# Optimization experiments

Measured on AMD Instinct MI355X. Metric: run time of the kernel, lower is better.

The kernel has to match this reference:

```python
import jax, jax.numpy as jnp
import numpy as np

PREV_SIZE = 1024
SIZE = 4096
BATCH = 8192


def setup_inputs() -> dict:
    key = jax.random.key(0)
    k1, k2, k3, k4 = jax.random.split(key, 4)
    return {
        "prev_layer_output": jax.random.normal(k1, (PREV_SIZE, BATCH), dtype=jnp.float32),
        "input_A_weights": jax.random.normal(k2, (SIZE, PREV_SIZE), dtype=jnp.float32),
        "input_B_weights": jax.random.normal(k3, (SIZE, PREV_SIZE), dtype=jnp.float32),
        "table_weights": jax.random.normal(k4, (16, SIZE), dtype=jnp.float32),
    }


def reference(prev_layer_output, input_A_weights, input_B_weights, table_weights):
    # Soft input selection via row-softmax over previous neurons.
    pa = jax.nn.softmax(input_A_weights, axis=1)   # (size, prev_size)
    pb = jax.nn.softmax(input_B_weights, axis=1)   # (size, prev_size)
    pt = jax.nn.softmax(table_weights, axis=0)     # (16, size) softmax over gates

    A = pa @ prev_layer_output                     # (size, batch)
    B = pb @ prev_layer_output                     # (size, batch)
    AB = A * B

    p = pt[:, :, None]                             # (16, size, 1) broadcast over batch
    # Fused weighted sum over the 16 soft logic gates (no (16,size,batch) buffer).
    out = (
        p[1] * AB
        + p[2] * (A - AB)
        + p[3] * A
        + p[4] * (B - AB)
        + p[5] * B
        + p[6] * (A + B - 2.0 * AB)
        + p[7] * (A + B - AB)
        + p[8] * (1.0 - (A + B - AB))
        + p[9] * (1.0 - (A + B - 2.0 * AB))
        + p[10] * (1.0 - B)
        + p[11] * (1.0 - B + AB)
        + p[12] * (1.0 - A)
        + p[13] * (1.0 - A + AB)
        + p[14] * (1.0 - AB)
        + p[15]
    )
    return out
```

## Files before the change

### kernel.cpp

```cpp
#include <hip/hip_runtime.h>
#include <hip/hip_bf16.h>

#define K_DIM 1024
#define M_DIM 4096
#define N_DIM 8192
#define BK 32
#define PAD 40

typedef __attribute__((ext_vector_type(8))) __bf16 bf16x8_t;
typedef __attribute__((ext_vector_type(4))) float f32x4;
typedef __attribute__((ext_vector_type(4))) int i32x4;

__device__ inline unsigned short f2bf(float f) {
    unsigned u = __float_as_uint(f);
    u += 0x7FFF + ((u >> 16) & 1);
    return (unsigned short)(u >> 16);
}

__global__ void row_softmax_kernel(const float* __restrict__ w,
                                   unsigned short* __restrict__ o) {
    const int row = blockIdx.x;
    const int tid = threadIdx.x;
    const float4 v = reinterpret_cast<const float4*>(w + (size_t)row * K_DIM)[tid];
    float m = fmaxf(fmaxf(v.x, v.y), fmaxf(v.z, v.w));
    #pragma unroll
    for (int off = 32; off >= 1; off >>= 1) m = fmaxf(m, __shfl_xor(m, off));
    __shared__ float redm[4];
    __shared__ float reds[4];
    if ((tid & 63) == 0) redm[tid >> 6] = m;
    __syncthreads();
    m = fmaxf(fmaxf(redm[0], redm[1]), fmaxf(redm[2], redm[3]));
    const float e0 = __expf(v.x - m), e1 = __expf(v.y - m);
    const float e2 = __expf(v.z - m), e3 = __expf(v.w - m);
    float s = e0 + e1 + e2 + e3;
    #pragma unroll
    for (int off = 32; off >= 1; off >>= 1) s += __shfl_xor(s, off);
    if ((tid & 63) == 0) reds[tid >> 6] = s;
    __syncthreads();
    s = reds[0] + reds[1] + reds[2] + reds[3];
    const float inv = 1.0f / s;
    ushort4 r;
    r.x = f2bf(e0 * inv); r.y = f2bf(e1 * inv);
    r.z = f2bf(e2 * inv); r.w = f2bf(e3 * inv);
    reinterpret_cast<ushort4*>(o + (size_t)row * K_DIM)[tid] = r;
}

__global__ void transpose_conv_kernel(const float* __restrict__ src,
                                      unsigned short* __restrict__ dst) {
    __shared__ float t[32][33];
    const int n0 = blockIdx.x * 32;
    const int k0 = blockIdx.y * 32;
    const int tx = threadIdx.x, ty = threadIdx.y;
    #pragma unroll
    for (int i = ty; i < 32; i += 8)
        t[i][tx] = src[(size_t)(k0 + i) * N_DIM + n0 + tx];
    __syncthreads();
    #pragma unroll
    for (int i = ty; i < 32; i += 8)
        dst[(size_t)(n0 + i) * K_DIM + k0 + tx] = f2bf(t[tx][i]);
}

__global__ void coef_kernel(const float* __restrict__ tw,
                            float4* __restrict__ coef) {
    const int r = blockIdx.x * 256 + threadIdx.x;
    float p[16];
    float m = -1e30f;
    #pragma unroll
    for (int k = 0; k < 16; ++k) { p[k] = tw[k * M_DIM + r]; m = fmaxf(m, p[k]); }
    float s = 0.f;
    #pragma unroll
    for (int k = 0; k < 16; ++k) { p[k] = __expf(p[k] - m); s += p[k]; }
    const float inv = 1.f / s;
    #pragma unroll
    for (int k = 0; k < 16; ++k) p[k] *= inv;
    const float cA  = p[2]+p[3]+p[6]+p[7]-p[8]-p[9]-p[12]-p[13];
    const float cB  = p[4]+p[5]+p[6]+p[7]-p[8]-p[9]-p[10]-p[11];
    const float cAB = p[1]-p[2]-p[4]-2.f*p[6]-p[7]+p[8]+2.f*p[9]+p[11]+p[13]-p[14];
    const float c0  = p[8]+p[9]+p[10]+p[11]+p[12]+p[13]+p[14]+p[15];
    coef[r] = make_float4(cA, cB, cAB, c0);
}

__global__ __launch_bounds__(256, 2)
void dual_gemm_kernel(const unsigned short* __restrict__ pa,
                      const unsigned short* __restrict__ pb,
                      const unsigned short* __restrict__ pv,
                      const float4* __restrict__ coef,
                      float* __restrict__ out) {
    __shared__ unsigned short sA[128 * PAD];
    __shared__ unsigned short sB[128 * PAD];
    __shared__ unsigned short sP[128 * PAD];

    const int tid = threadIdx.x;
    const int lane = tid & 63;
    const int wid = tid >> 6;
    const int wm = wid >> 1, wn = wid & 1;
    const int bm = blockIdx.y, bn = blockIdx.x;

    f32x4 accA[4][4], accB[4][4];
    const f32x4 z = {0.f, 0.f, 0.f, 0.f};
    #pragma unroll
    for (int i = 0; i < 4; ++i)
        #pragma unroll
        for (int j = 0; j < 4; ++j) { accA[i][j] = z; accB[i][j] = z; }

    const size_t a_base = (size_t)(bm * 128) * K_DIM;
    const size_t p_base = (size_t)(bn * 128) * K_DIM;

    const int frag_row = lane & 15;
    const int frag_k = (lane >> 4) * 8;

    for (int k0 = 0; k0 < K_DIM; k0 += BK) {
        __syncthreads();
        #pragma unroll
        for (int i = 0; i < 2; ++i) {
            const int c = tid + i * 256;
            const int r = c >> 2;
            const int kk = (c & 3) * 8;
            *reinterpret_cast<i32x4*>(&sA[r * PAD + kk]) =
                *reinterpret_cast<const i32x4*>(&pa[a_base + (size_t)r * K_DIM + k0 + kk]);
            *reinterpret_cast<i32x4*>(&sB[r * PAD + kk]) =
                *reinterpret_cast<const i32x4*>(&pb[a_base + (size_t)r * K_DIM + k0 + kk]);
            *reinterpret_cast<i32x4*>(&sP[r * PAD + kk]) =
                *reinterpret_cast<const i32x4*>(&pv[p_base + (size_t)r * K_DIM + k0 + kk]);
        }
        __syncthreads();

        bf16x8_t af[4], bfr[4], pf[4];
        #pragma unroll
        for (int mi = 0; mi < 4; ++mi) {
            const int row = wm * 64 + mi * 16 + frag_row;
            af[mi]  = *reinterpret_cast<const bf16x8_t*>(&sA[row * PAD + frag_k]);
            bfr[mi] = *reinterpret_cast<const bf16x8_t*>(&sB[row * PAD + frag_k]);
        }
        #pragma unroll
        for (int ni = 0; ni < 4; ++ni) {
            const int col = wn * 64 + ni * 16 + frag_row;
            pf[ni] = *reinterpret_cast<const bf16x8_t*>(&sP[col * PAD + frag_k]);
        }
        #pragma unroll
        for (int mi = 0; mi < 4; ++mi)
            #pragma unroll
            for (int ni = 0; ni < 4; ++ni) {
                accA[mi][ni] = __builtin_amdgcn_mfma_f32_16x16x32_bf16(
                    af[mi], pf[ni], accA[mi][ni], 0, 0, 0);
                accB[mi][ni] = __builtin_amdgcn_mfma_f32_16x16x32_bf16(
                    bfr[mi], pf[ni], accB[mi][ni], 0, 0, 0);
            }
    }

    const int row_grp = lane >> 4;
    #pragma unroll
    for (int mi = 0; mi < 4; ++mi) {
        #pragma unroll
        for (int ni = 0; ni < 4; ++ni) {
            const int gr0 = bm * 128 + wm * 64 + mi * 16 + row_grp * 4;
            const int gc  = bn * 128 + wn * 64 + ni * 16 + (lane & 15);
            #pragma unroll
            for (int i = 0; i < 4; ++i) {
                const int r = gr0 + i;
                const float4 cf = coef[r];
                const float av = accA[mi][ni][i];
                const float bv = accB[mi][ni][i];
                out[(size_t)r * N_DIM + gc] =
                    fmaf(cf.z, av * bv, fmaf(cf.x, av, fmaf(cf.y, bv, cf.w)));
            }
        }
    }
}

extern "C" void kernel_launch(void* const* d_in, const int* in_sizes, int n_in,
                              void* d_out, int out_size, void* d_ws, size_t ws_size,
                              hipStream_t stream) {
    const float* prev = (const float*)d_in[0];
    const float* wa   = (const float*)d_in[1];
    const float* wb   = (const float*)d_in[2];
    const float* tw   = (const float*)d_in[3];
    float* out = (float*)d_out;

    char* ws = (char*)d_ws;
    unsigned short* pa = (unsigned short*)ws;
    unsigned short* pb = (unsigned short*)(ws + 8388608);
    unsigned short* pv = (unsigned short*)(ws + 16777216);
    float4* coef       = (float4*)(ws + 33554432);

    row_softmax_kernel<<<M_DIM, 256, 0, stream>>>(wa, pa);
    row_softmax_kernel<<<M_DIM, 256, 0, stream>>>(wb, pb);
    transpose_conv_kernel<<<dim3(N_DIM / 32, K_DIM / 32), dim3(32, 8), 0, stream>>>(prev, pv);
    coef_kernel<<<M_DIM / 256, 256, 0, stream>>>(tw, coef);
    dual_gemm_kernel<<<dim3(N_DIM / 128, M_DIM / 128), 256, 0, stream>>>(pa, pb, pv, coef, out);
}
```

Measured before the change: 179.9 us.

## Load GEMM tiles with direct global-to-LDS copies, XOR swizzle, and BK=64

Replaces the register-staged global-to-shared tile copies with global_load_lds direct-to-LDS 16-byte loads. The shared-memory layout changes from padded rows to an XOR-swizzled 128-byte row layout to avoid bank conflicts. The K tile is doubled to 64, which halves the number of barrier pairs per K sweep. The change removes VGPR staging and load/store instruction overhead, but it relies on the per-wave LDS destination addressing of the builtin being correct and enlarges shared memory per block.

After: 150.2 us. 16.5% less time.

```diff
diff --git a/kernel.cpp b/kernel.cpp
--- a/kernel.cpp
+++ b/kernel.cpp
@@ -4,17 +4,21 @@
 #define K_DIM 1024
 #define M_DIM 4096
 #define N_DIM 8192
-#define BK 32
-#define PAD 40
+#define BK 64
 
 typedef __attribute__((ext_vector_type(8))) __bf16 bf16x8_t;
 typedef __attribute__((ext_vector_type(4))) float f32x4;
-typedef __attribute__((ext_vector_type(4))) int i32x4;
 
 __device__ inline unsigned short f2bf(float f) {
     unsigned u = __float_as_uint(f);
     u += 0x7FFF + ((u >> 16) & 1);
     return (unsigned short)(u >> 16);
+}
+
+__device__ __forceinline__ void gload_lds16(const void* g, void* l) {
+    __builtin_amdgcn_global_load_lds(
+        (const __attribute__((address_space(1))) unsigned int*)g,
+        (__attribute__((address_space(3))) unsigned int*)l, 16, 0, 0);
 }
 
 __global__ void row_softmax_kernel(const float* __restrict__ w,
@@ -86,9 +90,9 @@
                       const unsigned short* __restrict__ pv,
                       const float4* __restrict__ coef,
                       float* __restrict__ out) {
-    __shared__ unsigned short sA[128 * PAD];
-    __shared__ unsigned short sB[128 * PAD];
-    __shared__ unsigned short sP[128 * PAD];
+    __shared__ unsigned short sA[128 * BK];
+    __shared__ unsigned short sB[128 * BK];
+    __shared__ unsigned short sP[128 * BK];
 
     const int tid = threadIdx.x;
     const int lane = tid & 63;
@@ -103,49 +107,59 @@
         #pragma unroll
         for (int j = 0; j < 4; ++j) { accA[i][j] = z; accB[i][j] = z; }
 
-    const size_t a_base = (size_t)(bm * 128) * K_DIM;
-    const size_t p_base = (size_t)(bn * 128) * K_DIM;
+    const int sub_row = lane >> 3;
+    const int scol16  = (lane & 7) ^ sub_row;
 
     const int frag_row = lane & 15;
-    const int frag_k = (lane >> 4) * 8;
+    const int fk16base = lane >> 4;
 
     for (int k0 = 0; k0 < K_DIM; k0 += BK) {
         __syncthreads();
         #pragma unroll
-        for (int i = 0; i < 2; ++i) {
-            const int c = tid + i * 256;
-            const int r = c >> 2;
-            const int kk = (c & 3) * 8;
-            *reinterpret_cast<i32x4*>(&sA[r * PAD + kk]) =
-                *reinterpret_cast<const i32x4*>(&pa[a_base + (size_t)r * K_DIM + k0 + kk]);
-            *reinterpret_cast<i32x4*>(&sB[r * PAD + kk]) =
-                *reinterpret_cast<const i32x4*>(&pb[a_base + (size_t)r * K_DIM + k0 + kk]);
-            *reinterpret_cast<i32x4*>(&sP[r * PAD + kk]) =
-                *reinterpret_cast<const i32x4*>(&pv[p_base + (size_t)r * K_DIM + k0 + kk]);
+        for (int j = 0; j < 4; ++j) {
+            const int c   = wid * 4 + j;
+            const int row = c * 8 + sub_row;
+            const size_t goffA = (size_t)(bm * 128 + row) * K_DIM + k0;
+            const size_t goffP = (size_t)(bn * 128 + row) * K_DIM + k0;
+            const char* gA = (const char*)(pa + goffA) + scol16 * 16;
+            const char* gB = (const char*)(pb + goffA) + scol16 * 16;
+            const char* gP = (const char*)(pv + goffP) + scol16 * 16;
+            char* lA = (char*)sA + c * 1024;
+            char* lB = (char*)sB + c * 1024;
+            char* lP = (char*)sP + c * 1024;
+            gload_lds16(gA, lA);
+            gload_lds16(gB, lB);
+            gload_lds16(gP, lP);
         }
         __syncthreads();
 
-        bf16x8_t af[4], bfr[4], pf[4];
-        #pragma unroll
-        for (int mi = 0; mi < 4; ++mi) {
-            const int row = wm * 64 + mi * 16 + frag_row;
-            af[mi]  = *reinterpret_cast<const bf16x8_t*>(&sA[row * PAD + frag_k]);
-            bfr[mi] = *reinterpret_cast<const bf16x8_t*>(&sB[row * PAD + frag_k]);
+        #pragma unroll
+        for (int kk = 0; kk < 2; ++kk) {
+            bf16x8_t af[4], bfr[4], pf[4];
+            const int fk16 = fk16base + kk * 4;
+            #pragma unroll
+            for (int mi = 0; mi < 4; ++mi) {
+                const int row  = wm * 64 + mi * 16 + frag_row;
+                const int byte = row * 128 + ((fk16 ^ (row & 7)) * 16);
+                af[mi]  = *reinterpret_cast<const bf16x8_t*>((const char*)sA + byte);
+                bfr[mi] = *reinterpret_cast<const bf16x8_t*>((const char*)sB + byte);
+            }
+            #pragma unroll
+            for (int ni = 0; ni < 4; ++ni) {
+                const int col  = wn * 64 + ni * 16 + frag_row;
+                const int byte = col * 128 + ((fk16 ^ (col & 7)) * 16);
+                pf[ni] = *reinterpret_cast<const bf16x8_t*>((const char*)sP + byte);
+            }
+            #pragma unroll
+            for (int mi = 0; mi < 4; ++mi)
+                #pragma unroll
+                for (int ni = 0; ni < 4; ++ni) {
+                    accA[mi][ni] = __builtin_amdgcn_mfma_f32_16x16x32_bf16(
+                        af[mi], pf[ni], accA[mi][ni], 0, 0, 0);
+                    accB[mi][ni] = __builtin_amdgcn_mfma_f32_16x16x32_bf16(
+                        bfr[mi], pf[ni], accB[mi][ni], 0, 0, 0);
+                }
         }
-        #pragma unroll
-        for (int ni = 0; ni < 4; ++ni) {
-            const int col = wn * 64 + ni * 16 + frag_row;
-            pf[ni] = *reinterpret_cast<const bf16x8_t*>(&sP[col * PAD + frag_k]);
-        }
-        #pragma unroll
-        for (int mi = 0; mi < 4; ++mi)
-            #pragma unroll
-            for (int ni = 0; ni < 4; ++ni) {
-                accA[mi][ni] = __builtin_amdgcn_mfma_f32_16x16x32_bf16(
-                    af[mi], pf[ni], accA[mi][ni], 0, 0, 0);
-                accB[mi][ni] = __builtin_amdgcn_mfma_f32_16x16x32_bf16(
-                    bfr[mi], pf[ni], accB[mi][ni], 0, 0, 0);
-            }
     }
 
     const int row_grp = lane >> 4;
```

## Pipeline GEMM with triple-buffered direct-to-LDS loads and XOR-swizzled layout

Applied to the files above, without the earlier changes.

Rewrites the dual GEMM main loop to stage tiles with global_load_lds directly into a triple-buffered, XOR-swizzled LDS layout. Loads run two stages ahead, synchronised with explicit vmcnt/lgkmcnt waits and one barrier per iteration, and MFMA priority is raised. This is meant to hide global memory latency and remove register round-trips and bank conflicts. The two row-softmax launches are also merged into one. LDS use rises to 72KB, which may limit occupancy to two blocks per CU.

Measured after the change: 163.4 us. 1.1x faster.

```diff
diff --git a/kernel.cpp b/kernel.cpp
--- a/kernel.cpp
+++ b/kernel.cpp
@@ -5,11 +5,25 @@
 #define M_DIM 4096
 #define N_DIM 8192
 #define BK 32
-#define PAD 40
+#define BM 128
+#define BN 128
+#define NT 32
+
+#define OFF_A 0
+#define OFF_B 8192
+#define OFF_P 16384
+#define BUF_BYTES 24576
 
 typedef __attribute__((ext_vector_type(8))) __bf16 bf16x8_t;
 typedef __attribute__((ext_vector_type(4))) float f32x4;
-typedef __attribute__((ext_vector_type(4))) int i32x4;
+
+#define SBAR do { __builtin_amdgcn_sched_barrier(0); \
+                  __builtin_amdgcn_s_barrier(); \
+                  __builtin_amdgcn_sched_barrier(0); } while (0)
+#define LGKM0 do { asm volatile("s_waitcnt lgkmcnt(0)" ::: "memory"); \
+                   __builtin_amdgcn_sched_barrier(0); } while (0)
+#define VMCNT(n) do { asm volatile("s_waitcnt vmcnt(" #n ")" ::: "memory"); \
+                      __builtin_amdgcn_sched_barrier(0); } while (0)
 
 __device__ inline unsigned short f2bf(float f) {
     unsigned u = __float_as_uint(f);
@@ -17,9 +31,20 @@
     return (unsigned short)(u >> 16);
 }
 
-__global__ void row_softmax_kernel(const float* __restrict__ w,
-                                   unsigned short* __restrict__ o) {
-    const int row = blockIdx.x;
+__device__ __forceinline__ void gload_lds16(const void* g, void* l) {
+    __builtin_amdgcn_global_load_lds(
+        (const __attribute__((address_space(1))) unsigned int*)g,
+        (__attribute__((address_space(3))) unsigned int*)l, 16, 0, 0);
+}
+
+__global__ void dual_softmax_kernel(const float* __restrict__ wa,
+                                    const float* __restrict__ wb,
+                                    unsigned short* __restrict__ pa,
+                                    unsigned short* __restrict__ pb) {
+    const int idx = blockIdx.x;
+    const float* w = (idx < M_DIM) ? wa : wb;
+    unsigned short* o = (idx < M_DIM) ? pa : pb;
+    const int row = idx & (M_DIM - 1);
     const int tid = threadIdx.x;
     const float4 v = reinterpret_cast<const float4*>(w + (size_t)row * K_DIM)[tid];
     float m = fmaxf(fmaxf(v.x, v.y), fmaxf(v.z, v.w));
@@ -86,15 +111,29 @@
                       const unsigned short* __restrict__ pv,
                       const float4* __restrict__ coef,
                       float* __restrict__ out) {
-    __shared__ unsigned short sA[128 * PAD];
-    __shared__ unsigned short sB[128 * PAD];
-    __shared__ unsigned short sP[128 * PAD];
+    __shared__ unsigned short lds[3 * BUF_BYTES / 2];
 
     const int tid = threadIdx.x;
     const int lane = tid & 63;
-    const int wid = tid >> 6;
-    const int wm = wid >> 1, wn = wid & 1;
+    const int w = tid >> 6;
+    const int wm = w >> 1, wn = w & 1;
     const int bm = blockIdx.y, bn = blockIdx.x;
+
+    const int sub  = lane >> 2;
+    const int scol = (lane & 3) ^ ((lane >> 3) & 3);
+
+    const int c0 = w * 2, c1 = w * 2 + 1;
+    const char* sA0 = (const char*)pa + ((size_t)(bm * BM + c0 * 16 + sub) * K_DIM) * 2 + scol * 16;
+    const char* sA1 = (const char*)pa + ((size_t)(bm * BM + c1 * 16 + sub) * K_DIM) * 2 + scol * 16;
+    const char* sB0 = (const char*)pb + ((size_t)(bm * BM + c0 * 16 + sub) * K_DIM) * 2 + scol * 16;
+    const char* sB1 = (const char*)pb + ((size_t)(bm * BM + c1 * 16 + sub) * K_DIM) * 2 + scol * 16;
+    const char* sP0 = (const char*)pv + ((size_t)(bn * BN + c0 * 16 + sub) * K_DIM) * 2 + scol * 16;
+    const char* sP1 = (const char*)pv + ((size_t)(bn * BN + c1 * 16 + sub) * K_DIM) * 2 + scol * 16;
+
+    const int fr  = lane & 15;
+    const int fk  = lane >> 4;
+    const int arow0 = wm * 64 + fr;
+    const int prow0 = wn * 64 + fr;
 
     f32x4 accA[4][4], accB[4][4];
     const f32x4 z = {0.f, 0.f, 0.f, 0.f};
@@ -103,49 +142,79 @@
         #pragma unroll
         for (int j = 0; j < 4; ++j) { accA[i][j] = z; accB[i][j] = z; }
 
-    const size_t a_base = (size_t)(bm * 128) * K_DIM;
-    const size_t p_base = (size_t)(bn * 128) * K_DIM;
-
-    const int frag_row = lane & 15;
-    const int frag_k = (lane >> 4) * 8;
-
-    for (int k0 = 0; k0 < K_DIM; k0 += BK) {
-        __syncthreads();
-        #pragma unroll
-        for (int i = 0; i < 2; ++i) {
-            const int c = tid + i * 256;
-            const int r = c >> 2;
-            const int kk = (c & 3) * 8;
-            *reinterpret_cast<i32x4*>(&sA[r * PAD + kk]) =
-                *reinterpret_cast<const i32x4*>(&pa[a_base + (size_t)r * K_DIM + k0 + kk]);
-            *reinterpret_cast<i32x4*>(&sB[r * PAD + kk]) =
-                *reinterpret_cast<const i32x4*>(&pb[a_base + (size_t)r * K_DIM + k0 + kk]);
-            *reinterpret_cast<i32x4*>(&sP[r * PAD + kk]) =
-                *reinterpret_cast<const i32x4*>(&pv[p_base + (size_t)r * K_DIM + k0 + kk]);
+    #define STAGE_ALL(bo) do {                                              \
+        char* base = (char*)lds + (bo);                                     \
+        gload_lds16(sA0, base + OFF_A + c0 * 1024);                         \
+        gload_lds16(sA1, base + OFF_A + c1 * 1024);                         \
+        gload_lds16(sB0, base + OFF_B + c0 * 1024);                         \
+        gload_lds16(sB1, base + OFF_B + c1 * 1024);                         \
+        gload_lds16(sP0, base + OFF_P + c0 * 1024);                         \
+        gload_lds16(sP1, base + OFF_P + c1 * 1024);                         \
+        sA0 += BK * 2; sA1 += BK * 2; sB0 += BK * 2; sB1 += BK * 2;         \
+        sP0 += BK * 2; sP1 += BK * 2;                                       \
+    } while (0)
+
+    #define READ_FRAGS(bo)                                                   \
+        bf16x8_t af[4], bfv[4], pf[4];                                       \
+        {                                                                    \
+            const char* base = (const char*)lds + (bo);                      \
+            _Pragma("unroll")                                                \
+            for (int mi = 0; mi < 4; ++mi) {                                 \
+                const int row = arow0 + mi * 16;                             \
+                const int byte = row * 64 + ((fk ^ ((row >> 1) & 3)) << 4);  \
+                af[mi]  = *reinterpret_cast<const bf16x8_t*>(base + OFF_A + byte); \
+                bfv[mi] = *reinterpret_cast<const bf16x8_t*>(base + OFF_B + byte); \
+            }                                                                \
+            _Pragma("unroll")                                                \
+            for (int ni = 0; ni < 4; ++ni) {                                 \
+                const int row = prow0 + ni * 16;                             \
+                const int byte = row * 64 + ((fk ^ ((row >> 1) & 3)) << 4);  \
+                pf[ni] = *reinterpret_cast<const bf16x8_t*>(base + OFF_P + byte); \
+            }                                                                \
         }
-        __syncthreads();
-
-        bf16x8_t af[4], bfr[4], pf[4];
-        #pragma unroll
-        for (int mi = 0; mi < 4; ++mi) {
-            const int row = wm * 64 + mi * 16 + frag_row;
-            af[mi]  = *reinterpret_cast<const bf16x8_t*>(&sA[row * PAD + frag_k]);
-            bfr[mi] = *reinterpret_cast<const bf16x8_t*>(&sB[row * PAD + frag_k]);
-        }
-        #pragma unroll
-        for (int ni = 0; ni < 4; ++ni) {
-            const int col = wn * 64 + ni * 16 + frag_row;
-            pf[ni] = *reinterpret_cast<const bf16x8_t*>(&sP[col * PAD + frag_k]);
-        }
-        #pragma unroll
-        for (int mi = 0; mi < 4; ++mi)
-            #pragma unroll
-            for (int ni = 0; ni < 4; ++ni) {
-                accA[mi][ni] = __builtin_amdgcn_mfma_f32_16x16x32_bf16(
-                    af[mi], pf[ni], accA[mi][ni], 0, 0, 0);
-                accB[mi][ni] = __builtin_amdgcn_mfma_f32_16x16x32_bf16(
-                    bfr[mi], pf[ni], accB[mi][ni], 0, 0, 0);
-            }
+
+    #define MFMA_ALL do {                                                    \
+        __builtin_amdgcn_s_setprio(1);                                       \
+        _Pragma("unroll")                                                    \
+        for (int mi = 0; mi < 4; ++mi)                                       \
+            _Pragma("unroll")                                                \
+            for (int ni = 0; ni < 4; ++ni) {                                 \
+                accA[mi][ni] = __builtin_amdgcn_mfma_f32_16x16x32_bf16(      \
+                    af[mi], pf[ni], accA[mi][ni], 0, 0, 0);                  \
+                accB[mi][ni] = __builtin_amdgcn_mfma_f32_16x16x32_bf16(      \
+                    bfv[mi], pf[ni], accB[mi][ni], 0, 0, 0);                 \
+            }                                                                \
+        __builtin_amdgcn_s_setprio(0);                                       \
+    } while (0)
+
+    STAGE_ALL(0);
+    STAGE_ALL(BUF_BYTES);
+    VMCNT(6);
+    SBAR;
+
+    int curb = 0, stgb = 2 * BUF_BYTES;
+    for (int t = 0; t < NT - 2; ++t) {
+        STAGE_ALL(stgb);
+        READ_FRAGS(curb);
+        LGKM0;
+        MFMA_ALL;
+        VMCNT(6);
+        SBAR;
+        stgb = curb;
+        curb = (curb == 2 * BUF_BYTES) ? 0 : curb + BUF_BYTES;
+    }
+    {
+        READ_FRAGS(curb);
+        LGKM0;
+        MFMA_ALL;
+        VMCNT(0);
+        SBAR;
+        curb = (curb == 2 * BUF_BYTES) ? 0 : curb + BUF_BYTES;
+    }
+    {
+        READ_FRAGS(curb);
+        LGKM0;
+        MFMA_ALL;
     }
 
     const int row_grp = lane >> 4;
@@ -153,8 +222,8 @@
     for (int mi = 0; mi < 4; ++mi) {
         #pragma unroll
         for (int ni = 0; ni < 4; ++ni) {
-            const int gr0 = bm * 128 + wm * 64 + mi * 16 + row_grp * 4;
-            const int gc  = bn * 128 + wn * 64 + ni * 16 + (lane & 15);
+            const int gr0 = bm * BM + wm * 64 + mi * 16 + row_grp * 4;
+            const int gc  = bn * BN + wn * 64 + ni * 16 + (lane & 15);
             #pragma unroll
             for (int i = 0; i < 4; ++i) {
                 const int r = gr0 + i;
@@ -183,9 +252,8 @@
     unsigned short* pv = (unsigned short*)(ws + 16777216);
     float4* coef       = (float4*)(ws + 33554432);
 
-    row_softmax_kernel<<<M_DIM, 256, 0, stream>>>(wa, pa);
-    row_softmax_kernel<<<M_DIM, 256, 0, stream>>>(wb, pb);
+    dual_softmax_kernel<<<2 * M_DIM, 256, 0, stream>>>(wa, wb, pa, pb);
     transpose_conv_kernel<<<dim3(N_DIM / 32, K_DIM / 32), dim3(32, 8), 0, stream>>>(prev, pv);
     coef_kernel<<<M_DIM / 256, 256, 0, stream>>>(tw, coef);
-    dual_gemm_kernel<<<dim3(N_DIM / 128, M_DIM / 128), 256, 0, stream>>>(pa, pb, pv, coef, out);
-}
+    dual_gemm_kernel<<<dim3(N_DIM / BN, M_DIM / BM), 256, 0, stream>>>(pa, pb, pv, coef, out);
+}
```

## Double-buffer GEMM tiles via direct global-to-LDS loads with XOR swizzle

Applied to the files above, without the earlier changes.

The dual GEMM now stages tiles straight from global memory into LDS using global_load_lds, with two LDS buffers so the next k-tile loads while the current one feeds the MFMAs. An XOR swizzle replaces the padded layout to avoid bank conflicts, and s_setprio raises priority around the MFMA block. The two row-softmax launches are also merged into one kernel. This trades a more intricate sync scheme (vmcnt waits plus a barrier) and double the LDS footprint for fewer register round-trips and less exposed load latency.

Measured after the change: 164.0 us. 1.1x faster.

```diff
diff --git a/kernel.cpp b/kernel.cpp
--- a/kernel.cpp
+++ b/kernel.cpp
@@ -5,11 +5,20 @@
 #define M_DIM 4096
 #define N_DIM 8192
 #define BK 32
-#define PAD 40
+#define BM 128
+#define BN 128
+#define NT 32
+
+#define OFF_A 0
+#define OFF_B 8192
+#define OFF_P 16384
+#define BUF_BYTES 24576
 
 typedef __attribute__((ext_vector_type(8))) __bf16 bf16x8_t;
 typedef __attribute__((ext_vector_type(4))) float f32x4;
-typedef __attribute__((ext_vector_type(4))) int i32x4;
+
+#define SBAR __builtin_amdgcn_s_barrier()
+#define VMCNT0 asm volatile("s_waitcnt vmcnt(0)" ::: "memory")
 
 __device__ inline unsigned short f2bf(float f) {
     unsigned u = __float_as_uint(f);
@@ -17,9 +26,20 @@
     return (unsigned short)(u >> 16);
 }
 
-__global__ void row_softmax_kernel(const float* __restrict__ w,
-                                   unsigned short* __restrict__ o) {
-    const int row = blockIdx.x;
+__device__ __forceinline__ void gload_lds16(const void* g, void* l) {
+    __builtin_amdgcn_global_load_lds(
+        (const __attribute__((address_space(1))) unsigned int*)g,
+        (__attribute__((address_space(3))) unsigned int*)l, 16, 0, 0);
+}
+
+__global__ void dual_softmax_kernel(const float* __restrict__ wa,
+                                    const float* __restrict__ wb,
+                                    unsigned short* __restrict__ pa,
+                                    unsigned short* __restrict__ pb) {
+    const int idx = blockIdx.x;
+    const float* w = (idx < M_DIM) ? wa : wb;
+    unsigned short* o = (idx < M_DIM) ? pa : pb;
+    const int row = idx & (M_DIM - 1);
     const int tid = threadIdx.x;
     const float4 v = reinterpret_cast<const float4*>(w + (size_t)row * K_DIM)[tid];
     float m = fmaxf(fmaxf(v.x, v.y), fmaxf(v.z, v.w));
@@ -86,15 +106,36 @@
                       const unsigned short* __restrict__ pv,
                       const float4* __restrict__ coef,
                       float* __restrict__ out) {
-    __shared__ unsigned short sA[128 * PAD];
-    __shared__ unsigned short sB[128 * PAD];
-    __shared__ unsigned short sP[128 * PAD];
+    __shared__ unsigned short lds[2 * BUF_BYTES / 2];
 
     const int tid = threadIdx.x;
     const int lane = tid & 63;
-    const int wid = tid >> 6;
-    const int wm = wid >> 1, wn = wid & 1;
+    const int w = tid >> 6;
+    const int wm = w >> 1, wn = w & 1;
     const int bm = blockIdx.y, bn = blockIdx.x;
+
+    const int sub  = lane >> 2;
+    const int scol = (lane & 3) ^ ((lane >> 3) & 3);
+
+    const int c0 = 2 * w, c1 = 2 * w + 1;
+    const char* sA0 = (const char*)pa + ((size_t)(bm * BM + c0 * 16 + sub) * K_DIM) * 2 + scol * 16;
+    const char* sA1 = (const char*)pa + ((size_t)(bm * BM + c1 * 16 + sub) * K_DIM) * 2 + scol * 16;
+    const char* sB0 = (const char*)pb + ((size_t)(bm * BM + c0 * 16 + sub) * K_DIM) * 2 + scol * 16;
+    const char* sB1 = (const char*)pb + ((size_t)(bm * BM + c1 * 16 + sub) * K_DIM) * 2 + scol * 16;
+    const char* sP0 = (const char*)pv + ((size_t)(bn * BN + c0 * 16 + sub) * K_DIM) * 2 + scol * 16;
+    const char* sP1 = (const char*)pv + ((size_t)(bn * BN + c1 * 16 + sub) * K_DIM) * 2 + scol * 16;
+
+    const int fr = lane & 15;
+    const int fk = lane >> 4;
+
+    int aoff[4], poff[4];
+    #pragma unroll
+    for (int i = 0; i < 4; ++i) {
+        const int ar = wm * 64 + fr + i * 16;
+        aoff[i] = ar * 64 + ((fk ^ ((ar >> 1) & 3)) << 4);
+        const int pr = wn * 64 + fr + i * 16;
+        poff[i] = pr * 64 + ((fk ^ ((pr >> 1) & 3)) << 4);
+    }
 
     f32x4 accA[4][4], accB[4][4];
     const f32x4 z = {0.f, 0.f, 0.f, 0.f};
@@ -103,40 +144,38 @@
         #pragma unroll
         for (int j = 0; j < 4; ++j) { accA[i][j] = z; accB[i][j] = z; }
 
-    const size_t a_base = (size_t)(bm * 128) * K_DIM;
-    const size_t p_base = (size_t)(bn * 128) * K_DIM;
-
-    const int frag_row = lane & 15;
-    const int frag_k = (lane >> 4) * 8;
-
-    for (int k0 = 0; k0 < K_DIM; k0 += BK) {
-        __syncthreads();
-        #pragma unroll
-        for (int i = 0; i < 2; ++i) {
-            const int c = tid + i * 256;
-            const int r = c >> 2;
-            const int kk = (c & 3) * 8;
-            *reinterpret_cast<i32x4*>(&sA[r * PAD + kk]) =
-                *reinterpret_cast<const i32x4*>(&pa[a_base + (size_t)r * K_DIM + k0 + kk]);
-            *reinterpret_cast<i32x4*>(&sB[r * PAD + kk]) =
-                *reinterpret_cast<const i32x4*>(&pb[a_base + (size_t)r * K_DIM + k0 + kk]);
-            *reinterpret_cast<i32x4*>(&sP[r * PAD + kk]) =
-                *reinterpret_cast<const i32x4*>(&pv[p_base + (size_t)r * K_DIM + k0 + kk]);
+    #define STAGE_TO(buf_base) do {                                          \
+        char* base = (char*)(buf_base);                                      \
+        gload_lds16(sA0, base + OFF_A + c0 * 1024);                          \
+        gload_lds16(sA1, base + OFF_A + c1 * 1024);                          \
+        gload_lds16(sB0, base + OFF_B + c0 * 1024);                          \
+        gload_lds16(sB1, base + OFF_B + c1 * 1024);                          \
+        gload_lds16(sP0, base + OFF_P + c0 * 1024);                          \
+        gload_lds16(sP1, base + OFF_P + c1 * 1024);                          \
+        sA0 += BK * 2; sA1 += BK * 2; sB0 += BK * 2; sB1 += BK * 2;          \
+        sP0 += BK * 2; sP1 += BK * 2;                                        \
+    } while (0)
+
+    char* buf0 = (char*)lds;
+    char* buf1 = (char*)lds + BUF_BYTES;
+
+    STAGE_TO(buf0);
+    VMCNT0;
+    SBAR;
+
+    for (int t = 0; t < NT; ++t) {
+        const bool more = (t < NT - 1);
+        if (more) STAGE_TO(buf1);
+
+        bf16x8_t af[4], bfv[4], pf[4];
+        #pragma unroll
+        for (int i = 0; i < 4; ++i) {
+            af[i]  = *reinterpret_cast<const bf16x8_t*>(buf0 + OFF_A + aoff[i]);
+            bfv[i] = *reinterpret_cast<const bf16x8_t*>(buf0 + OFF_B + aoff[i]);
+            pf[i]  = *reinterpret_cast<const bf16x8_t*>(buf0 + OFF_P + poff[i]);
         }
-        __syncthreads();
-
-        bf16x8_t af[4], bfr[4], pf[4];
-        #pragma unroll
-        for (int mi = 0; mi < 4; ++mi) {
-            const int row = wm * 64 + mi * 16 + frag_row;
-            af[mi]  = *reinterpret_cast<const bf16x8_t*>(&sA[row * PAD + frag_k]);
-            bfr[mi] = *reinterpret_cast<const bf16x8_t*>(&sB[row * PAD + frag_k]);
-        }
-        #pragma unroll
-        for (int ni = 0; ni < 4; ++ni) {
-            const int col = wn * 64 + ni * 16 + frag_row;
-            pf[ni] = *reinterpret_cast<const bf16x8_t*>(&sP[col * PAD + frag_k]);
-        }
+
+        __builtin_amdgcn_s_setprio(1);
         #pragma unroll
         for (int mi = 0; mi < 4; ++mi)
             #pragma unroll
@@ -144,8 +183,15 @@
                 accA[mi][ni] = __builtin_amdgcn_mfma_f32_16x16x32_bf16(
                     af[mi], pf[ni], accA[mi][ni], 0, 0, 0);
                 accB[mi][ni] = __builtin_amdgcn_mfma_f32_16x16x32_bf16(
-                    bfr[mi], pf[ni], accB[mi][ni], 0, 0, 0);
+                    bfv[mi], pf[ni], accB[mi][ni], 0, 0, 0);
             }
+        __builtin_amdgcn_s_setprio(0);
+
+        if (more) {
+            VMCNT0;
+            SBAR;
+        }
+        char* tmp = buf0; buf0 = buf1; buf1 = tmp;
     }
 
     const int row_grp = lane >> 4;
@@ -153,8 +199,8 @@
     for (int mi = 0; mi < 4; ++mi) {
         #pragma unroll
         for (int ni = 0; ni < 4; ++ni) {
-            const int gr0 = bm * 128 + wm * 64 + mi * 16 + row_grp * 4;
-            const int gc  = bn * 128 + wn * 64 + ni * 16 + (lane & 15);
+            const int gr0 = bm * BM + wm * 64 + mi * 16 + row_grp * 4;
+            const int gc  = bn * BN + wn * 64 + ni * 16 + (lane & 15);
             #pragma unroll
             for (int i = 0; i < 4; ++i) {
                 const int r = gr0 + i;
@@ -183,9 +229,8 @@
     unsigned short* pv = (unsigned short*)(ws + 16777216);
     float4* coef       = (float4*)(ws + 33554432);
 
-    row_softmax_kernel<<<M_DIM, 256, 0, stream>>>(wa, pa);
-    row_softmax_kernel<<<M_DIM, 256, 0, stream>>>(wb, pb);
+    dual_softmax_kernel<<<2 * M_DIM, 256, 0, stream>>>(wa, wb, pa, pb);
     transpose_conv_kernel<<<dim3(N_DIM / 32, K_DIM / 32), dim3(32, 8), 0, stream>>>(prev, pv);
     coef_kernel<<<M_DIM / 256, 256, 0, stream>>>(tw, coef);
-    dual_gemm_kernel<<<dim3(N_DIM / 128, M_DIM / 128), 256, 0, stream>>>(pa, pb, pv, coef, out);
-}
+    dual_gemm_kernel<<<dim3(N_DIM / BN, M_DIM / BM), 256, 0, stream>>>(pa, pb, pv, coef, out);
+}
```
